# Optimization experiments

Hardware: AMD Instinct MI355X
Metric: run time of the kernel (lower is better)

The kernel has to match this reference:

```python
import jax, jax.numpy as jnp
import numpy as np

L, N, E, H, R = 2048, 4, 768, 12, 16
ALPHA = 16.0
LORA_SCALE = ALPHA / R
HEAD_DIM = E // H


def setup_inputs() -> dict:
    rng = jax.random.key(0)
    ks = jax.random.split(rng, 15)
    g = lambda i, shape, s=1.0: jax.random.normal(ks[i], shape, jnp.float32) * s
    return {
        "query": g(0, (L, N, E)),
        "key": g(1, (L, N, E)),
        "value": g(2, (L, N, E)),
        "in_proj_weight": g(3, (3 * E, E), 0.02),
        "in_proj_bias": g(4, (3 * E,), 0.02),
        "q_down": g(5, (R, E), 0.02),
        "q_up": g(6, (E, R), 0.02),
        "k_down": g(7, (R, E), 0.02),
        "k_up": g(8, (E, R), 0.02),
        "v_down": g(9, (R, E), 0.02),
        "v_up": g(10, (E, R), 0.02),
        "out_proj_weight": g(11, (E, E), 0.02),
        "out_proj_bias": g(12, (E,), 0.02),
        "out_down": g(13, (R, E), 0.02),
        "out_up": g(14, (E, R), 0.02),
    }


def _lora_linear(x, W, b, down, up):
    # y = x W^T + b + scale * (x down^T) up^T   (LoRA-adapted nn.Linear)
    return x @ W.T + b + LORA_SCALE * ((x @ down.T) @ up.T)


def reference(query, key, value, in_proj_weight, in_proj_bias,
              q_down, q_up, k_down, k_up, v_down, v_up,
              out_proj_weight, out_proj_bias, out_down, out_up):
    Wq, Wk, Wv = jnp.split(in_proj_weight, 3, axis=0)
    bq, bk, bv = jnp.split(in_proj_bias, 3)
    q = _lora_linear(query, Wq, bq, q_down, q_up)   # (L,N,E)
    k = _lora_linear(key, Wk, bk, k_down, k_up)     # (S,N,E)
    v = _lora_linear(value, Wv, bv, v_down, v_up)

    def to_heads(t):  # (T,N,E) -> (N,H,T,hd)
        return t.reshape(t.shape[0], N, H, HEAD_DIM).transpose(1, 2, 0, 3)

    qh, kh, vh = to_heads(q), to_heads(k), to_heads(v)
    scale = 1.0 / jnp.sqrt(jnp.float32(HEAD_DIM))
    scores = jnp.einsum('nhld,nhsd->nhls', qh * scale, kh)  # (N,H,L,S)
    attn = jax.nn.softmax(scores, axis=-1)
    o = jnp.einsum('nhls,nhsd->nhld', attn, vh)             # (N,H,L,hd)
    o = o.transpose(2, 0, 1, 3).reshape(L, N, E)            # (L,N,E)
    return _lora_linear(o, out_proj_weight, out_proj_bias, out_down, out_up)
```

## Files before the change

kernel.cpp:

```cpp
#include <hip/hip_runtime.h>

#define LL 2048
#define NN 4
#define EE 768
#define HH 12
#define RR 16
#define HD 64
#define TT (LL*NN)
#define F3 (3*EE)
#define KA 832

typedef __bf16 bf16;
typedef bf16 bf16x4 __attribute__((ext_vector_type(4)));
typedef bf16 bf16x8 __attribute__((ext_vector_type(8)));
typedef float floatx4 __attribute__((ext_vector_type(4)));

__global__ __launch_bounds__(256) void cast_x(
    const float* __restrict__ q, const float* __restrict__ k,
    const float* __restrict__ v, bf16* __restrict__ Xa)
{
    const int bid = blockIdx.x;
    const int third = bid / (TT/8);
    const int r0 = (bid % (TT/8)) * 8;
    const float* x = (third == 0) ? q : (third == 1) ? k : v;
    const int tid = threadIdx.x;
    #pragma unroll
    for (int i = 0; i < 6; ++i) {
        const int e4 = i*256 + tid;
        const int row = e4 / 192;
        const int col = (e4 % 192) * 4;
        const float4 f = *(const float4*)(x + (size_t)(r0+row)*EE + col);
        bf16x4 h = { (bf16)f.x, (bf16)f.y, (bf16)f.z, (bf16)f.w };
        *(bf16x4*)(Xa + ((size_t)third*TT + r0 + row)*KA + col) = h;
    }
}

__global__ __launch_bounds__(256) void prep_w(
    const float* __restrict__ W,  const float* __restrict__ qu,
    const float* __restrict__ ku, const float* __restrict__ vu,
    const float* __restrict__ Wo, const float* __restrict__ ou,
    const float* __restrict__ qd, const float* __restrict__ kd,
    const float* __restrict__ vd, const float* __restrict__ odw,
    bf16* __restrict__ Wa, bf16* __restrict__ Dm)
{
    const int f = blockIdx.x;
    const int tid = threadIdx.x;
    if (f < 3072) {
        const float* src;
        const float* up;
        if (f < F3) {
            const int third = f / EE, fe = f % EE;
            src = W + (size_t)f*EE;
            up  = ((third == 0) ? qu : (third == 1) ? ku : vu) + fe*RR;
        } else {
            const int fe = f - F3;
            src = Wo + (size_t)fe*EE;
            up  = ou + fe*RR;
        }
        bf16* row = Wa + (size_t)f*KA;
        #pragma unroll
        for (int i = 0; i < 3; ++i)
            row[i*256 + tid] = (bf16)src[i*256 + tid];
        if (tid < 64)
            row[EE + tid] = (tid < RR) ? (bf16)up[tid] : (bf16)0.f;
    } else {
        const int f2 = f - 3072;
        const int which = f2 >> 4, r = f2 & 15;
        const float* dsrc = (which == 0) ? qd : (which == 1) ? kd
                          : (which == 2) ? vd : odw;
        bf16* drow = Dm + (size_t)f2*EE;
        #pragma unroll
        for (int i = 0; i < 3; ++i)
            drow[i*256 + tid] = (bf16)dsrc[(size_t)r*EE + i*256 + tid];
    }
}

template<int XA>
__global__ __launch_bounds__(256) void lora_rank16(
    bf16* __restrict__ A, const bf16* __restrict__ Dm)
{
    __shared__ float red[4][64][16];
    const int row0 = blockIdx.x * 64;
    const int dn = XA ? (row0 >> 13) : 3;
    const bf16* D = Dm + (size_t)dn*16*EE;
    const int tid = threadIdx.x;
    const int wave = tid >> 6, lane = tid & 63;
    const int quad = lane >> 4, l16 = lane & 15;

    floatx4 acc[4];
    #pragma unroll
    for (int rt = 0; rt < 4; ++rt) acc[rt] = (floatx4){0.f,0.f,0.f,0.f};

    #pragma unroll
    for (int ks = 0; ks < 6; ++ks) {
        const int k0 = wave*192 + ks*32;
        const bf16x8 b = *(const bf16x8*)(D + (size_t)l16*EE + k0 + quad*8);
        #pragma unroll
        for (int rt = 0; rt < 4; ++rt) {
            const bf16x8 a = *(const bf16x8*)(
                A + (size_t)(row0 + rt*16 + l16)*KA + k0 + quad*8);
            acc[rt] = __builtin_amdgcn_mfma_f32_16x16x32_bf16(a, b, acc[rt], 0, 0, 0);
        }
    }

    #pragma unroll
    for (int rt = 0; rt < 4; ++rt)
        #pragma unroll
        for (int rr = 0; rr < 4; ++rr)
            red[wave][rt*16 + quad*4 + rr][l16] = acc[rt][rr];
    __syncthreads();

    {
        const int row = tid >> 2, cq = (tid & 3) * 4;
        bf16x4 o;
        #pragma unroll
        for (int j = 0; j < 4; ++j) {
            const float s = red[0][row][cq+j] + red[1][row][cq+j]
                          + red[2][row][cq+j] + red[3][row][cq+j];
            o[j] = (bf16)s;
        }
        *(bf16x4*)(A + (size_t)(row0+row)*KA + EE + cq) = o;
    }
    #pragma unroll
    for (int p = 0; p < 3; ++p) {
        const int id = p*256 + tid;
        const int row = id / 12, c = id % 12;
        *(bf16x4*)(A + (size_t)(row0+row)*KA + 784 + c*4) = (bf16x4){};
    }
}

template<int MODE>
__global__ __launch_bounds__(256) void gemm_aug(
    const bf16* __restrict__ A,
    const bf16* __restrict__ B,
    const float* __restrict__ bias,
    bf16* __restrict__ qo, bf16* __restrict__ ko, bf16* __restrict__ vo,
    float* __restrict__ fo)
{
    __shared__ bf16 As[128][72];
    __shared__ bf16 Bs[128][72];
    const int t0 = blockIdx.x * 128;
    const int f0 = blockIdx.y * 128;
    const int tid = threadIdx.x;
    const int wave = tid >> 6, lane = tid & 63;
    const int quad = lane >> 4, l16 = lane & 15;
    const int m0 = (wave & 1) * 64;
    const int n0 = (wave >> 1) * 64;

    const int third = (MODE == 0) ? (f0 / EE) : 0;
    const bf16* Aeff = (MODE == 0) ? (A + (size_t)third*TT*KA) : A;

    floatx4 acc[4][4];
    #pragma unroll
    for (int rt = 0; rt < 4; ++rt)
        #pragma unroll
        for (int ct = 0; ct < 4; ++ct) acc[rt][ct] = (floatx4){0.f,0.f,0.f,0.f};

    for (int kb = 0; kb < KA/64; ++kb) {
        __syncthreads();
        #pragma unroll
        for (int c = 0; c < 4; ++c) {
            int id = c*256 + tid;
            int row = id >> 3, cg = id & 7;
            *(bf16x8*)(&As[row][cg*8]) =
                *(const bf16x8*)(Aeff + (size_t)(t0+row)*KA + kb*64 + cg*8);
            *(bf16x8*)(&Bs[row][cg*8]) =
                *(const bf16x8*)(B + (size_t)(f0+row)*KA + kb*64 + cg*8);
        }
        __syncthreads();
        #pragma unroll
        for (int kc = 0; kc < 2; ++kc) {
            bf16x8 a[4], bfr[4];
            #pragma unroll
            for (int rt = 0; rt < 4; ++rt)
                a[rt] = *(const bf16x8*)(&As[m0 + rt*16 + l16][kc*32 + quad*8]);
            #pragma unroll
            for (int ct = 0; ct < 4; ++ct)
                bfr[ct] = *(const bf16x8*)(&Bs[n0 + ct*16 + l16][kc*32 + quad*8]);
            #pragma unroll
            for (int rt = 0; rt < 4; ++rt)
                #pragma unroll
                for (int ct = 0; ct < 4; ++ct)
                    acc[rt][ct] = __builtin_amdgcn_mfma_f32_16x16x32_bf16(
                        a[rt], bfr[ct], acc[rt][ct], 0, 0, 0);
        }
    }

    #pragma unroll
    for (int rt = 0; rt < 4; ++rt) {
        #pragma unroll
        for (int r = 0; r < 4; ++r) {
            const int t = t0 + m0 + rt*16 + quad*4 + r;
            #pragma unroll
            for (int ct = 0; ct < 4; ++ct) {
                const int fl = n0 + ct*16 + l16;
                float c = acc[rt][ct][r] + bias[f0 + fl];
                if (MODE == 0) {
                    const int fe = (f0 % EE) + fl;
                    const int h = fe >> 6, d = fe & 63;
                    const int l = t >> 2, n = t & 3;
                    const size_t idx = (((size_t)(n*HH + h)*LL) + l)*HD + d;
                    if (third == 0)      qo[idx] = (bf16)(c * 0.180336877f);
                    else if (third == 1) ko[idx] = (bf16)c;
                    else                 vo[idx] = (bf16)c;
                } else {
                    fo[(size_t)t*EE + f0 + fl] = c;
                }
            }
        }
    }
}

__global__ __launch_bounds__(256) void vtrans(
    const bf16* __restrict__ vin, bf16* __restrict__ vout)
{
    __shared__ bf16 T[64][64];
    const int nh = blockIdx.x >> 5;
    const int l0 = (blockIdx.x & 31) * 64;
    const int tid = threadIdx.x;
    const bf16* src = vin + ((size_t)nh*LL + l0)*HD;
    #pragma unroll
    for (int c = 0; c < 2; ++c) {
        int id = c*256 + tid;
        int row = id >> 3, dg = id & 7;
        int pg = dg ^ (row & 7);
        *(bf16x8*)(&T[row][pg*8]) = *(const bf16x8*)(src + row*HD + dg*8);
    }
    __syncthreads();
    bf16* dst = vout + (size_t)nh*HD*LL;
    const int wave = tid >> 6, lane = tid & 63;
    #pragma unroll
    for (int it = 0; it < 2; ++it) {
        const int d  = it*32 + wave*8 + (lane >> 3);
        const int cg = lane & 7;
        bf16x8 vv;
        #pragma unroll
        for (int j = 0; j < 8; ++j) {
            const int lrow = cg*8 + j;
            const int pg = (d >> 3) ^ (lrow & 7);
            vv[j] = T[lrow][pg*8 + (d & 7)];
        }
        *(bf16x8*)(dst + (size_t)d*LL + l0 + cg*8) = vv;
    }
}

__global__ __launch_bounds__(256) void attn_mfma(
    const bf16* __restrict__ qf, const bf16* __restrict__ kf,
    const bf16* __restrict__ vf, bf16* __restrict__ Oa)
{
    __shared__ bf16 Ks[64][72];
    __shared__ bf16 Vt[64][72];
    __shared__ bf16 Ps[128][72];

    const int bid = blockIdx.x;
    const int nh = bid % 48;
    const int l0 = (bid / 48) * 128;
    const int tid  = threadIdx.x;
    const int wave = tid >> 6;
    const int lane = tid & 63;
    const int quad = lane >> 4;
    const int l16  = lane & 15;
    const int m0   = wave * 32;

    const bf16* qb = qf + (size_t)nh * LL * HD;
    const bf16* kb = kf + (size_t)nh * LL * HD;
    const bf16* vb = vf + (size_t)nh * HD * LL;

    bf16x8 aq[2][2];
    #pragma unroll
    for (int kc = 0; kc < 2; ++kc)
        #pragma unroll
        for (int rt = 0; rt < 2; ++rt)
            aq[kc][rt] = *(const bf16x8*)(
                qb + (size_t)(l0 + m0 + rt*16 + l16)*HD + kc*32 + quad*8);

    floatx4 oacc[2][4];
    float lrow[2][4];
    #pragma unroll
    for (int rt = 0; rt < 2; ++rt)
        #pragma unroll
        for (int ct = 0; ct < 4; ++ct) oacc[rt][ct] = (floatx4){0.f,0.f,0.f,0.f};
    #pragma unroll
    for (int rt = 0; rt < 2; ++rt)
        #pragma unroll
        for (int r = 0; r < 4; ++r) lrow[rt][r] = 0.f;

    for (int s0 = 0; s0 < LL; s0 += 64) {
        __syncthreads();
        #pragma unroll
        for (int it = 0; it < 2; ++it) {
            int lin  = it*256 + tid;
            int row  = lin >> 3;
            int colg = (lin & 7) * 8;
            *(bf16x8*)(&Ks[row][colg]) =
                *(const bf16x8*)(kb + (size_t)(s0+row)*HD + colg);
            *(bf16x8*)(&Vt[row][colg]) =
                *(const bf16x8*)(vb + (size_t)row*LL + s0 + colg);
        }
        __syncthreads();

        floatx4 sf[2][4];
        #pragma unroll
        for (int rt = 0; rt < 2; ++rt)
            #pragma unroll
            for (int ct = 0; ct < 4; ++ct) sf[rt][ct] = (floatx4){0.f,0.f,0.f,0.f};
        #pragma unroll
        for (int kc = 0; kc < 2; ++kc) {
            bf16x8 bk[4];
            #pragma unroll
            for (int ct = 0; ct < 4; ++ct)
                bk[ct] = *(const bf16x8*)(&Ks[ct*16 + l16][kc*32 + quad*8]);
            #pragma unroll
            for (int rt = 0; rt < 2; ++rt)
                #pragma unroll
                for (int ct = 0; ct < 4; ++ct)
                    sf[rt][ct] = __builtin_amdgcn_mfma_f32_16x16x32_bf16(
                        aq[kc][rt], bk[ct], sf[rt][ct], 0, 0, 0);
        }

        #pragma unroll
        for (int rt = 0; rt < 2; ++rt) {
            #pragma unroll
            for (int r = 0; r < 4; ++r) {
                const int prow = m0 + rt*16 + quad*4 + r;
                float ps = 0.f;
                #pragma unroll
                for (int ct = 0; ct < 4; ++ct) {
                    const float p = __builtin_exp2f(sf[rt][ct][r]);
                    Ps[prow][ct*16 + l16] = (bf16)p;
                    ps += p;
                }
                lrow[rt][r] += ps;
            }
        }

        #pragma unroll
        for (int kc = 0; kc < 2; ++kc) {
            bf16x8 ap[2], bv[4];
            ap[0] = *(const bf16x8*)(&Ps[m0      + l16][kc*32 + quad*8]);
            ap[1] = *(const bf16x8*)(&Ps[m0 + 16 + l16][kc*32 + quad*8]);
            #pragma unroll
            for (int ct = 0; ct < 4; ++ct)
                bv[ct] = *(const bf16x8*)(&Vt[ct*16 + l16][kc*32 + quad*8]);
            #pragma unroll
            for (int rt = 0; rt < 2; ++rt)
                #pragma unroll
                for (int ct = 0; ct < 4; ++ct)
                    oacc[rt][ct] = __builtin_amdgcn_mfma_f32_16x16x32_bf16(
                        ap[rt], bv[ct], oacc[rt][ct], 0, 0, 0);
        }
    }

    #pragma unroll
    for (int rt = 0; rt < 2; ++rt)
        #pragma unroll
        for (int r = 0; r < 4; ++r) {
            float s = lrow[rt][r];
            #pragma unroll
            for (int off = 1; off < 16; off <<= 1)
                s += __shfl_xor(s, off, 64);
            lrow[rt][r] = s;
        }

    const int n = nh / HH, h = nh % HH;
    #pragma unroll
    for (int rt = 0; rt < 2; ++rt) {
        #pragma unroll
        for (int r = 0; r < 4; ++r) {
            const float inv = 1.f / lrow[rt][r];
            const int lq = l0 + m0 + rt*16 + quad*4 + r;
            const size_t t = (size_t)lq*NN + n;
            #pragma unroll
            for (int ct = 0; ct < 4; ++ct)
                Oa[t*KA + h*64 + ct*16 + l16] = (bf16)(oacc[rt][ct][r] * inv);
        }
    }
}

extern "C" void kernel_launch(void* const* d_in, const int* in_sizes, int n_in,
                              void* d_out, int out_size, void* d_ws, size_t ws_size,
                              hipStream_t stream) {
    const float* q   = (const float*)d_in[0];
    const float* k   = (const float*)d_in[1];
    const float* v   = (const float*)d_in[2];
    const float* W   = (const float*)d_in[3];
    const float* b   = (const float*)d_in[4];
    const float* qd  = (const float*)d_in[5];
    const float* qu  = (const float*)d_in[6];
    const float* kd  = (const float*)d_in[7];
    const float* ku  = (const float*)d_in[8];
    const float* vd  = (const float*)d_in[9];
    const float* vu  = (const float*)d_in[10];
    const float* Wo  = (const float*)d_in[11];
    const float* bo  = (const float*)d_in[12];
    const float* odw = (const float*)d_in[13];
    const float* ou  = (const float*)d_in[14];
    float* out = (float*)d_out;

    char* wsb = (char*)d_ws;
    bf16* Xa  = (bf16*)wsb;
    bf16* vfb = (bf16*)wsb;
    bf16* Oa  = (bf16*)(wsb + (size_t)TT*EE*2);
    bf16* Wa  = (bf16*)(wsb + (size_t)3*TT*KA*2);
    bf16* qfb = (bf16*)((char*)Wa + (size_t)3072*KA*2);
    bf16* kfb = qfb + (size_t)TT*EE;
    bf16* vld = kfb + (size_t)TT*EE;
    bf16* Dm  = vld + (size_t)TT*EE;

    cast_x<<<3072, 256, 0, stream>>>(q, k, v, Xa);
    prep_w<<<3136, 256, 0, stream>>>(W, qu, ku, vu, Wo, ou, qd, kd, vd, odw, Wa, Dm);
    lora_rank16<1><<<3*TT/64, 256, 0, stream>>>(Xa, Dm);
    gemm_aug<0><<<dim3(TT/128, F3/128), 256, 0, stream>>>(
        Xa, Wa, b, qfb, kfb, vld, nullptr);
    vtrans<<<48*32, 256, 0, stream>>>(vld, vfb);
    attn_mfma<<<48*16, 256, 0, stream>>>(qfb, kfb, vfb, Oa);
    lora_rank16<0><<<TT/64, 256, 0, stream>>>(Oa, Dm);
    gemm_aug<1><<<dim3(TT/128, EE/128), 256, 0, stream>>>(
        Oa, Wa + (size_t)F3*KA, bo, nullptr, nullptr, nullptr, out);
}
```

Before: 326.3 us.

## Halve attention query tile to 64 rows and XOR-swizzle K/V shared memory

```diff
diff --git a/kernel.cpp b/kernel.cpp
--- a/kernel.cpp
+++ b/kernel.cpp
@@ -248,132 +248,113 @@
     const bf16* __restrict__ qf, const bf16* __restrict__ kf,
     const bf16* __restrict__ vf, bf16* __restrict__ Oa)
 {
-    __shared__ bf16 Ks[64][72];
-    __shared__ bf16 Vt[64][72];
-    __shared__ bf16 Ps[128][72];
+    __shared__ bf16 Ks[64][64];
+    __shared__ bf16 Vt[64][64];
+    __shared__ bf16 Ps[64][72];
 
     const int bid = blockIdx.x;
     const int nh = bid % 48;
-    const int l0 = (bid / 48) * 128;
+    const int l0 = (bid / 48) * 64;
     const int tid  = threadIdx.x;
     const int wave = tid >> 6;
     const int lane = tid & 63;
     const int quad = lane >> 4;
     const int l16  = lane & 15;
-    const int m0   = wave * 32;
+    const int m0   = wave * 16;
+    const int lsw  = l16 & 7;
 
     const bf16* qb = qf + (size_t)nh * LL * HD;
     const bf16* kb = kf + (size_t)nh * LL * HD;
     const bf16* vb = vf + (size_t)nh * HD * LL;
 
-    bf16x8 aq[2][2];
+    bf16x8 aq[2];
     #pragma unroll
     for (int kc = 0; kc < 2; ++kc)
-        #pragma unroll
-        for (int rt = 0; rt < 2; ++rt)
-            aq[kc][rt] = *(const bf16x8*)(
-                qb + (size_t)(l0 + m0 + rt*16 + l16)*HD + kc*32 + quad*8);
-
-    floatx4 oacc[2][4];
-    float lrow[2][4];
-    #pragma unroll
-    for (int rt = 0; rt < 2; ++rt)
-        #pragma unroll
-        for (int ct = 0; ct < 4; ++ct) oacc[rt][ct] = (floatx4){0.f,0.f,0.f,0.f};
-    #pragma unroll
-    for (int rt = 0; rt < 2; ++rt)
-        #pragma unroll
-        for (int r = 0; r < 4; ++r) lrow[rt][r] = 0.f;
+        aq[kc] = *(const bf16x8*)(
+            qb + (size_t)(l0 + m0 + l16)*HD + kc*32 + quad*8);
+
+    floatx4 oacc[4];
+    float lrow[4];
+    #pragma unroll
+    for (int ct = 0; ct < 4; ++ct) oacc[ct] = (floatx4){0.f,0.f,0.f,0.f};
+    #pragma unroll
+    for (int r = 0; r < 4; ++r) lrow[r] = 0.f;
 
     for (int s0 = 0; s0 < LL; s0 += 64) {
         __syncthreads();
         #pragma unroll
         for (int it = 0; it < 2; ++it) {
-            int lin  = it*256 + tid;
-            int row  = lin >> 3;
-            int colg = (lin & 7) * 8;
-            *(bf16x8*)(&Ks[row][colg]) =
-                *(const bf16x8*)(kb + (size_t)(s0+row)*HD + colg);
-            *(bf16x8*)(&Vt[row][colg]) =
-                *(const bf16x8*)(vb + (size_t)row*LL + s0 + colg);
+            const int lin = it*256 + tid;
+            const int row = lin >> 3;
+            const int cg  = lin & 7;
+            const int sg  = cg ^ (row & 7);
+            *(bf16x8*)(&Ks[row][sg*8]) =
+                *(const bf16x8*)(kb + (size_t)(s0+row)*HD + cg*8);
+            *(bf16x8*)(&Vt[row][sg*8]) =
+                *(const bf16x8*)(vb + (size_t)row*LL + s0 + cg*8);
         }
         __syncthreads();
 
-        floatx4 sf[2][4];
-        #pragma unroll
-        for (int rt = 0; rt < 2; ++rt)
-            #pragma unroll
-            for (int ct = 0; ct < 4; ++ct) sf[rt][ct] = (floatx4){0.f,0.f,0.f,0.f};
+        floatx4 sf[4];
+        #pragma unroll
+        for (int ct = 0; ct < 4; ++ct) sf[ct] = (floatx4){0.f,0.f,0.f,0.f};
         #pragma unroll
         for (int kc = 0; kc < 2; ++kc) {
             bf16x8 bk[4];
             #pragma unroll
             for (int ct = 0; ct < 4; ++ct)
-                bk[ct] = *(const bf16x8*)(&Ks[ct*16 + l16][kc*32 + quad*8]);
-            #pragma unroll
-            for (int rt = 0; rt < 2; ++rt)
-                #pragma unroll
-                for (int ct = 0; ct < 4; ++ct)
-                    sf[rt][ct] = __builtin_amdgcn_mfma_f32_16x16x32_bf16(
-                        aq[kc][rt], bk[ct], sf[rt][ct], 0, 0, 0);
-        }
-
-        #pragma unroll
-        for (int rt = 0; rt < 2; ++rt) {
-            #pragma unroll
-            for (int r = 0; r < 4; ++r) {
-                const int prow = m0 + rt*16 + quad*4 + r;
-                float ps = 0.f;
-                #pragma unroll
-                for (int ct = 0; ct < 4; ++ct) {
-                    const float p = __builtin_exp2f(sf[rt][ct][r]);
-                    Ps[prow][ct*16 + l16] = (bf16)p;
-                    ps += p;
-                }
-                lrow[rt][r] += ps;
+                bk[ct] = *(const bf16x8*)(&Ks[ct*16 + l16][((kc*4+quad)^lsw)*8]);
+            #pragma unroll
+            for (int ct = 0; ct < 4; ++ct)
+                sf[ct] = __builtin_amdgcn_mfma_f32_16x16x32_bf16(
+                    aq[kc], bk[ct], sf[ct], 0, 0, 0);
+        }
+
+        #pragma unroll
+        for (int r = 0; r < 4; ++r) {
+            const int prow = m0 + quad*4 + r;
+            float ps = 0.f;
+            #pragma unroll
+            for (int ct = 0; ct < 4; ++ct) {
+                const float p = __builtin_exp2f(sf[ct][r]);
+                Ps[prow][ct*16 + l16] = (bf16)p;
+                ps += p;
             }
+            lrow[r] += ps;
         }
 
         #pragma unroll
         for (int kc = 0; kc < 2; ++kc) {
-            bf16x8 ap[2], bv[4];
-            ap[0] = *(const bf16x8*)(&Ps[m0      + l16][kc*32 + quad*8]);
-            ap[1] = *(const bf16x8*)(&Ps[m0 + 16 + l16][kc*32 + quad*8]);
+            const bf16x8 ap = *(const bf16x8*)(&Ps[m0 + l16][kc*32 + quad*8]);
+            bf16x8 bv[4];
             #pragma unroll
             for (int ct = 0; ct < 4; ++ct)
-                bv[ct] = *(const bf16x8*)(&Vt[ct*16 + l16][kc*32 + quad*8]);
-            #pragma unroll
-            for (int rt = 0; rt < 2; ++rt)
-                #pragma unroll
-                for (int ct = 0; ct < 4; ++ct)
-                    oacc[rt][ct] = __builtin_amdgcn_mfma_f32_16x16x32_bf16(
-                        ap[rt], bv[ct], oacc[rt][ct], 0, 0, 0);
-        }
-    }
-
-    #pragma unroll
-    for (int rt = 0; rt < 2; ++rt)
-        #pragma unroll
-        for (int r = 0; r < 4; ++r) {
-            float s = lrow[rt][r];
-            #pragma unroll
-            for (int off = 1; off < 16; off <<= 1)
-                s += __shfl_xor(s, off, 64);
-            lrow[rt][r] = s;
-        }
+                bv[ct] = *(const bf16x8*)(&Vt[ct*16 + l16][((kc*4+quad)^lsw)*8]);
+            #pragma unroll
+            for (int ct = 0; ct < 4; ++ct)
+                oacc[ct] = __builtin_amdgcn_mfma_f32_16x16x32_bf16(
+                    ap, bv[ct], oacc[ct], 0, 0, 0);
+        }
+    }
+
+    #pragma unroll
+    for (int r = 0; r < 4; ++r) {
+        float s = lrow[r];
+        #pragma unroll
+        for (int off = 1; off < 16; off <<= 1)
+            s += __shfl_xor(s, off, 64);
+        lrow[r] = s;
+    }
 
     const int n = nh / HH, h = nh % HH;
     #pragma unroll
-    for (int rt = 0; rt < 2; ++rt) {
-        #pragma unroll
-        for (int r = 0; r < 4; ++r) {
-            const float inv = 1.f / lrow[rt][r];
-            const int lq = l0 + m0 + rt*16 + quad*4 + r;
-            const size_t t = (size_t)lq*NN + n;
-            #pragma unroll
-            for (int ct = 0; ct < 4; ++ct)
-                Oa[t*KA + h*64 + ct*16 + l16] = (bf16)(oacc[rt][ct][r] * inv);
-        }
+    for (int r = 0; r < 4; ++r) {
+        const float inv = 1.f / lrow[r];
+        const int lq = l0 + m0 + quad*4 + r;
+        const size_t t = (size_t)lq*NN + n;
+        #pragma unroll
+        for (int ct = 0; ct < 4; ++ct)
+            Oa[t*KA + h*64 + ct*16 + l16] = (bf16)(oacc[ct][r] * inv);
     }
 }
 
@@ -413,7 +394,7 @@
     gemm_aug<0><<<dim3(TT/128, F3/128), 256, 0, stream>>>(
         Xa, Wa, b, qfb, kfb, vld, nullptr);
     vtrans<<<48*32, 256, 0, stream>>>(vld, vfb);
-    attn_mfma<<<48*16, 256, 0, stream>>>(qfb, kfb, vfb, Oa);
+    attn_mfma<<<48*32, 256, 0, stream>>>(qfb, kfb, vfb, Oa);
     lora_rank16<0><<<TT/64, 256, 0, stream>>>(Oa, Dm);
     gemm_aug<1><<<dim3(TT/128, EE/128), 256, 0, stream>>>(
         Oa, Wa + (size_t)F3*KA, bo, nullptr, nullptr, nullptr, out);
```

Measured after the change: 366.9 us. +12.5%, slower.
